# Kernel tuning notes

Hardware: AMD Instinct MI355X
Metric: run time of the kernel (lower is better)

Reference implementation:

```python
import jax, jax.numpy as jnp
import numpy as np

TOP_K = 4  # moe_top_k


def setup_inputs() -> dict:
    key = jax.random.key(0)
    k1, k2 = jax.random.split(key)
    # hidden states [B, S, D]
    x = jax.random.normal(k1, (4, 4096, 6144), dtype=jnp.float32)
    # router weight [D, E] (nnx.Linear kernel, no bias)
    W = jax.random.normal(k2, (6144, 16), dtype=jnp.float32) * 0.02
    return {"x": x, "W": W}


def reference(x, W):
    # logits: [B, S, E] -- promote to fp32 as the module does
    logits = jnp.einsum('bsd,de->bse', x.astype(jnp.float32), W.astype(jnp.float32))
    weights = jax.nn.softmax(logits, axis=-1)
    # top-k expert selection
    top_weights, top_experts = jax.lax.top_k(weights, TOP_K)
    # moe_normalize_expert_weights = 1 -> L1 normalize the selected weights
    top_weights = top_weights / jnp.sum(jnp.abs(top_weights), axis=-1, keepdims=True)
    return (weights.astype(x.dtype), top_weights.astype(x.dtype), top_experts)
```

## Files before the change

kernel.cpp:

```cpp
#include <hip/hip_runtime.h>
#include <cmath>


namespace {
constexpr int TOKENS = 16384;
constexpr int DIM    = 6144;
constexpr int NE     = 16;
constexpr int TOPK   = 4;
constexpr int T_TILE = 64;
constexpr int SUPER  = 128;
constexpr int RS     = 130;
constexpr int RPAD   = 20;
constexpr int TOPW_OFF = TOKENS * NE;
constexpr int EXP_OFF  = TOPW_OFF + TOKENS * TOPK;
}

__device__ __forceinline__ void fma16(float xs, const float* __restrict__ wrow,
                                      float (&ac)[NE]) {
    const float4 w0 = *reinterpret_cast<const float4*>(wrow + 0);
    const float4 w1 = *reinterpret_cast<const float4*>(wrow + 4);
    const float4 w2 = *reinterpret_cast<const float4*>(wrow + 8);
    const float4 w3 = *reinterpret_cast<const float4*>(wrow + 12);
    ac[0]  = fmaf(xs, w0.x, ac[0]);  ac[1]  = fmaf(xs, w0.y, ac[1]);
    ac[2]  = fmaf(xs, w0.z, ac[2]);  ac[3]  = fmaf(xs, w0.w, ac[3]);
    ac[4]  = fmaf(xs, w1.x, ac[4]);  ac[5]  = fmaf(xs, w1.y, ac[5]);
    ac[6]  = fmaf(xs, w1.z, ac[6]);  ac[7]  = fmaf(xs, w1.w, ac[7]);
    ac[8]  = fmaf(xs, w2.x, ac[8]);  ac[9]  = fmaf(xs, w2.y, ac[9]);
    ac[10] = fmaf(xs, w2.z, ac[10]); ac[11] = fmaf(xs, w2.w, ac[11]);
    ac[12] = fmaf(xs, w3.x, ac[12]); ac[13] = fmaf(xs, w3.y, ac[13]);
    ac[14] = fmaf(xs, w3.z, ac[14]); ac[15] = fmaf(xs, w3.w, ac[15]);
}

template <int KSLICES>
__global__ __launch_bounds__(256) void router_partial_kernel(
    const float* __restrict__ x, const float* __restrict__ W,
    float* __restrict__ partial)
{
    constexpr int KS = DIM / KSLICES;
    constexpr int NS = KS / SUPER;

    __shared__ float smem[T_TILE * RS];

    const int tid  = threadIdx.x;
    const int lane = tid & 63;
    const int wv   = tid >> 6;
    const int wvu  = __builtin_amdgcn_readfirstlane(wv);
    const int slice = blockIdx.x % KSLICES;
    const int tile  = blockIdx.x / KSLICES;
    const int t0 = tile * T_TILE;
    const int d0 = slice * KS;

    const int srow = wv * 2 + (lane >> 5);
    const int scol = (lane & 31) * 4;
    const float* xb = x + (size_t)(t0 + srow) * DIM + d0 + scol;

    float acc[NE];
    #pragma unroll
    for (int e = 0; e < NE; ++e) acc[e] = 0.f;

    float4 buf[8];
    #pragma unroll
    for (int i = 0; i < 8; ++i)
        buf[i] = *reinterpret_cast<const float4*>(xb + (size_t)(i * 8) * DIM);

    #pragma unroll 1
    for (int s = 0; s < NS; ++s) {
        #pragma unroll
        for (int i = 0; i < 8; ++i) {
            float* dst = &smem[(size_t)(srow + i * 8) * RS + scol];
            *reinterpret_cast<float2*>(dst)     = make_float2(buf[i].x, buf[i].y);
            *reinterpret_cast<float2*>(dst + 2) = make_float2(buf[i].z, buf[i].w);
        }
        if (s + 1 < NS) {
            const float* xn = xb + (size_t)(s + 1) * SUPER;
            #pragma unroll
            for (int i = 0; i < 8; ++i)
                buf[i] = *reinterpret_cast<const float4*>(xn + (size_t)(i * 8) * DIM);
        }
        __syncthreads();
        {
            const float* xr = &smem[(size_t)lane * RS + wvu * 32];
            const float* wp = W + (size_t)(d0 + s * SUPER + wvu * 32) * NE;
            #pragma unroll
            for (int q = 0; q < 16; ++q) {
                const float2 xq = *reinterpret_cast<const float2*>(xr + 2 * q);
                fma16(xq.x, wp + (2 * q) * NE, acc);
                fma16(xq.y, wp + (2 * q + 1) * NE, acc);
            }
        }
        __syncthreads();
    }

    #pragma unroll
    for (int q = 0; q < 4; ++q)
        *reinterpret_cast<float4*>(&smem[(size_t)(wvu * 64 + lane) * RPAD + 4 * q]) =
            make_float4(acc[4 * q], acc[4 * q + 1], acc[4 * q + 2], acc[4 * q + 3]);
    __syncthreads();

    if (wv == 0) {
        float4 r0[4];
        #pragma unroll
        for (int q = 0; q < 4; ++q)
            r0[q] = *reinterpret_cast<const float4*>(&smem[(size_t)lane * RPAD + 4 * q]);
        #pragma unroll
        for (int w = 1; w < 4; ++w) {
            #pragma unroll
            for (int q = 0; q < 4; ++q) {
                const float4 rw = *reinterpret_cast<const float4*>(
                    &smem[(size_t)(w * 64 + lane) * RPAD + 4 * q]);
                r0[q].x += rw.x; r0[q].y += rw.y; r0[q].z += rw.z; r0[q].w += rw.w;
            }
        }
        float* p = partial + ((size_t)slice * TOKENS + t0 + lane) * NE;
        #pragma unroll
        for (int q = 0; q < 4; ++q)
            *reinterpret_cast<float4*>(p + 4 * q) = r0[q];
    }
}

template <int KSLICES>
__global__ __launch_bounds__(128) void router_finish_kernel(
    const float* __restrict__ partial, float* __restrict__ out)
{
    const int t = blockIdx.x * 128 + threadIdx.x;
    float l[NE];
    {
        const float4* p0 = reinterpret_cast<const float4*>(partial + (size_t)t * NE);
        float4 a0 = p0[0], a1 = p0[1], a2 = p0[2], a3 = p0[3];
        #pragma unroll
        for (int s = 1; s < KSLICES; ++s) {
            const float4* q = reinterpret_cast<const float4*>(
                partial + ((size_t)s * TOKENS + t) * NE);
            float4 b0 = q[0], b1 = q[1], b2 = q[2], b3 = q[3];
            a0.x += b0.x; a0.y += b0.y; a0.z += b0.z; a0.w += b0.w;
            a1.x += b1.x; a1.y += b1.y; a1.z += b1.z; a1.w += b1.w;
            a2.x += b2.x; a2.y += b2.y; a2.z += b2.z; a2.w += b2.w;
            a3.x += b3.x; a3.y += b3.y; a3.z += b3.z; a3.w += b3.w;
        }
        l[0]=a0.x; l[1]=a0.y; l[2]=a0.z; l[3]=a0.w;
        l[4]=a1.x; l[5]=a1.y; l[6]=a1.z; l[7]=a1.w;
        l[8]=a2.x; l[9]=a2.y; l[10]=a2.z; l[11]=a2.w;
        l[12]=a3.x; l[13]=a3.y; l[14]=a3.z; l[15]=a3.w;
    }
    float mx = l[0];
    #pragma unroll
    for (int e = 1; e < NE; ++e) mx = fmaxf(mx, l[e]);
    float w[NE];
    float sum = 0.f;
    #pragma unroll
    for (int e = 0; e < NE; ++e) { w[e] = expf(l[e] - mx); sum += w[e]; }
    const float inv = 1.f / sum;
    #pragma unroll
    for (int e = 0; e < NE; ++e) w[e] *= inv;

    int   idx[TOPK];
    float tw[TOPK];
    unsigned used = 0;
    #pragma unroll
    for (int k = 0; k < TOPK; ++k) {
        float best = -1.f;
        int   bi   = 0;
        #pragma unroll
        for (int e = 0; e < NE; ++e) {
            const bool avail = ((used >> e) & 1u) == 0u;
            if (avail && w[e] > best) { best = w[e]; bi = e; }
        }
        used |= (1u << bi);
        idx[k] = bi;
        tw[k]  = best;
    }
    const float s4 = tw[0] + tw[1] + tw[2] + tw[3];
    const float rinv = 1.f / s4;

    float4* o0 = reinterpret_cast<float4*>(out + (size_t)t * NE);
    o0[0] = make_float4(w[0], w[1], w[2], w[3]);
    o0[1] = make_float4(w[4], w[5], w[6], w[7]);
    o0[2] = make_float4(w[8], w[9], w[10], w[11]);
    o0[3] = make_float4(w[12], w[13], w[14], w[15]);
    *reinterpret_cast<float4*>(out + TOPW_OFF + (size_t)t * TOPK) =
        make_float4(tw[0] * rinv, tw[1] * rinv, tw[2] * rinv, tw[3] * rinv);
    *reinterpret_cast<float4*>(out + EXP_OFF + (size_t)t * TOPK) =
        make_float4((float)idx[0], (float)idx[1], (float)idx[2], (float)idx[3]);
}

template <int KSLICES>
static void launch_impl(const float* x, const float* W, float* out, float* ws,
                        hipStream_t stream)
{
    const int blocks = 256 * KSLICES;
    router_partial_kernel<KSLICES><<<blocks, 256, 0, stream>>>(x, W, ws);
    router_finish_kernel<KSLICES><<<TOKENS / 128, 128, 0, stream>>>(ws, out);
}

extern "C" void kernel_launch(void* const* d_in, const int* in_sizes, int n_in,
                              void* d_out, int out_size, void* d_ws, size_t ws_size,
                              hipStream_t stream) {
    const float* x = (const float*)d_in[0];
    const float* W = (const float*)d_in[1];
    float* out = (float*)d_out;
    float* ws  = (float*)d_ws;

    const size_t per_slice = (size_t)TOKENS * NE * sizeof(float);
    if (ws_size >= 4 * per_slice) {
        launch_impl<4>(x, W, out, ws, stream);
    } else if (ws_size >= 2 * per_slice) {
        launch_impl<2>(x, W, out, ws, stream);
    } else {
        launch_impl<1>(x, W, out, ws, stream);
    }
}
```

Before: 90.10 us.

## Fuse split-K finish into partial kernel via last-block atomic counter

The separate finish kernel is replaced by a per-tile atomic counter, so the last of the four K-slice blocks sums the partials and runs softmax and top-k in the same launch. A small zero-counters kernel is added first. Loads of x become nontemporal to avoid polluting the cache, and the LDS row stride changes from 130 to 134. This relies on threadfence ordering for correctness and still issues two launches.

New measurement: 157.9 us. 1.75x slower.

```diff
diff --git a/kernel.cpp b/kernel.cpp
--- a/kernel.cpp
+++ b/kernel.cpp
@@ -9,10 +9,18 @@
 constexpr int TOPK   = 4;
 constexpr int T_TILE = 64;
 constexpr int SUPER  = 128;
-constexpr int RS     = 130;
+constexpr int RS     = 134;
 constexpr int RPAD   = 20;
+constexpr int KSL    = 4;
+constexpr int NTILES = TOKENS / T_TILE;
 constexpr int TOPW_OFF = TOKENS * NE;
 constexpr int EXP_OFF  = TOPW_OFF + TOKENS * TOPK;
+}
+
+typedef float f4 __attribute__((ext_vector_type(4)));
+
+__device__ __forceinline__ f4 ntload4(const float* p) {
+    return __builtin_nontemporal_load(reinterpret_cast<const f4*>(p));
 }
 
 __device__ __forceinline__ void fma16(float xs, const float* __restrict__ wrow,
@@ -31,22 +39,70 @@
     ac[14] = fmaf(xs, w3.z, ac[14]); ac[15] = fmaf(xs, w3.w, ac[15]);
 }
 
-template <int KSLICES>
-__global__ __launch_bounds__(256) void router_partial_kernel(
+__device__ __forceinline__ void finish_token(const float (&l)[NE], int tt,
+                                             float* __restrict__ out) {
+    float mx = l[0];
+    #pragma unroll
+    for (int e = 1; e < NE; ++e) mx = fmaxf(mx, l[e]);
+    float w[NE];
+    float sum = 0.f;
+    #pragma unroll
+    for (int e = 0; e < NE; ++e) { w[e] = expf(l[e] - mx); sum += w[e]; }
+    const float inv = 1.f / sum;
+    #pragma unroll
+    for (int e = 0; e < NE; ++e) w[e] *= inv;
+
+    int   idx[TOPK];
+    float tw[TOPK];
+    unsigned used = 0;
+    #pragma unroll
+    for (int k = 0; k < TOPK; ++k) {
+        float best = -1.f;
+        int   bi   = 0;
+        #pragma unroll
+        for (int e = 0; e < NE; ++e) {
+            const bool avail = ((used >> e) & 1u) == 0u;
+            if (avail && w[e] > best) { best = w[e]; bi = e; }
+        }
+        used |= (1u << bi);
+        idx[k] = bi;
+        tw[k]  = best;
+    }
+    const float s4 = tw[0] + tw[1] + tw[2] + tw[3];
+    const float rinv = 1.f / s4;
+
+    float4* o0 = reinterpret_cast<float4*>(out + (size_t)tt * NE);
+    o0[0] = make_float4(w[0], w[1], w[2], w[3]);
+    o0[1] = make_float4(w[4], w[5], w[6], w[7]);
+    o0[2] = make_float4(w[8], w[9], w[10], w[11]);
+    o0[3] = make_float4(w[12], w[13], w[14], w[15]);
+    *reinterpret_cast<float4*>(out + TOPW_OFF + (size_t)tt * TOPK) =
+        make_float4(tw[0] * rinv, tw[1] * rinv, tw[2] * rinv, tw[3] * rinv);
+    *reinterpret_cast<float4*>(out + EXP_OFF + (size_t)tt * TOPK) =
+        make_float4((float)idx[0], (float)idx[1], (float)idx[2], (float)idx[3]);
+}
+
+__global__ void zero_counters_kernel(int* __restrict__ cnt) {
+    cnt[threadIdx.x] = 0;
+}
+
+__global__ __launch_bounds__(256) void router_fused_partial_kernel(
     const float* __restrict__ x, const float* __restrict__ W,
-    float* __restrict__ partial)
+    float* __restrict__ partial, int* __restrict__ cnt,
+    float* __restrict__ out)
 {
-    constexpr int KS = DIM / KSLICES;
+    constexpr int KS = DIM / KSL;
     constexpr int NS = KS / SUPER;
 
     __shared__ float smem[T_TILE * RS];
+    __shared__ int sflag;
 
     const int tid  = threadIdx.x;
     const int lane = tid & 63;
     const int wv   = tid >> 6;
     const int wvu  = __builtin_amdgcn_readfirstlane(wv);
-    const int slice = blockIdx.x % KSLICES;
-    const int tile  = blockIdx.x / KSLICES;
+    const int slice = blockIdx.x & 3;
+    const int tile  = blockIdx.x >> 2;
     const int t0 = tile * T_TILE;
     const int d0 = slice * KS;
 
@@ -58,10 +114,10 @@
     #pragma unroll
     for (int e = 0; e < NE; ++e) acc[e] = 0.f;
 
-    float4 buf[8];
+    f4 buf[8];
     #pragma unroll
     for (int i = 0; i < 8; ++i)
-        buf[i] = *reinterpret_cast<const float4*>(xb + (size_t)(i * 8) * DIM);
+        buf[i] = ntload4(xb + (size_t)(i * 8) * DIM);
 
     #pragma unroll 1
     for (int s = 0; s < NS; ++s) {
@@ -75,7 +131,7 @@
             const float* xn = xb + (size_t)(s + 1) * SUPER;
             #pragma unroll
             for (int i = 0; i < 8; ++i)
-                buf[i] = *reinterpret_cast<const float4*>(xn + (size_t)(i * 8) * DIM);
+                buf[i] = ntload4(xn + (size_t)(i * 8) * DIM);
         }
         __syncthreads();
         {
@@ -115,11 +171,113 @@
         #pragma unroll
         for (int q = 0; q < 4; ++q)
             *reinterpret_cast<float4*>(p + 4 * q) = r0[q];
-    }
-}
-
-template <int KSLICES>
-__global__ __launch_bounds__(128) void router_finish_kernel(
+
+        __threadfence();
+        if (lane == 0) sflag = atomicAdd(&cnt[tile], 1);
+    }
+    __syncthreads();
+
+    if (sflag == 3 && tid < T_TILE) {
+        __threadfence();
+        const int t = t0 + tid;
+        float l[NE];
+        {
+            const float4* p0 = reinterpret_cast<const float4*>(partial + (size_t)t * NE);
+            float4 a0 = p0[0], a1 = p0[1], a2 = p0[2], a3 = p0[3];
+            #pragma unroll
+            for (int s = 1; s < KSL; ++s) {
+                const float4* q = reinterpret_cast<const float4*>(
+                    partial + ((size_t)s * TOKENS + t) * NE);
+                float4 b0 = q[0], b1 = q[1], b2 = q[2], b3 = q[3];
+                a0.x += b0.x; a0.y += b0.y; a0.z += b0.z; a0.w += b0.w;
+                a1.x += b1.x; a1.y += b1.y; a1.z += b1.z; a1.w += b1.w;
+                a2.x += b2.x; a2.y += b2.y; a2.z += b2.z; a2.w += b2.w;
+                a3.x += b3.x; a3.y += b3.y; a3.z += b3.z; a3.w += b3.w;
+            }
+            l[0]=a0.x; l[1]=a0.y; l[2]=a0.z; l[3]=a0.w;
+            l[4]=a1.x; l[5]=a1.y; l[6]=a1.z; l[7]=a1.w;
+            l[8]=a2.x; l[9]=a2.y; l[10]=a2.z; l[11]=a2.w;
+            l[12]=a3.x; l[13]=a3.y; l[14]=a3.z; l[15]=a3.w;
+        }
+        finish_token(l, t, out);
+    }
+}
+
+__global__ __launch_bounds__(256) void router_partial_sep_kernel(
+    const float* __restrict__ x, const float* __restrict__ W,
+    float* __restrict__ partial)
+{
+    constexpr int KS = DIM / KSL;
+    constexpr int NS = KS / SUPER;
+    __shared__ float smem[T_TILE * RS];
+    const int tid  = threadIdx.x;
+    const int lane = tid & 63;
+    const int wv   = tid >> 6;
+    const int wvu  = __builtin_amdgcn_readfirstlane(wv);
+    const int slice = blockIdx.x & 3;
+    const int tile  = blockIdx.x >> 2;
+    const int t0 = tile * T_TILE;
+    const int d0 = slice * KS;
+    const int srow = wv * 2 + (lane >> 5);
+    const int scol = (lane & 31) * 4;
+    const float* xb = x + (size_t)(t0 + srow) * DIM + d0 + scol;
+    float acc[NE];
+    #pragma unroll
+    for (int e = 0; e < NE; ++e) acc[e] = 0.f;
+    f4 buf[8];
+    #pragma unroll
+    for (int i = 0; i < 8; ++i) buf[i] = ntload4(xb + (size_t)(i * 8) * DIM);
+    #pragma unroll 1
+    for (int s = 0; s < NS; ++s) {
+        #pragma unroll
+        for (int i = 0; i < 8; ++i) {
+            float* dst = &smem[(size_t)(srow + i * 8) * RS + scol];
+            *reinterpret_cast<float2*>(dst)     = make_float2(buf[i].x, buf[i].y);
+            *reinterpret_cast<float2*>(dst + 2) = make_float2(buf[i].z, buf[i].w);
+        }
+        if (s + 1 < NS) {
+            const float* xn = xb + (size_t)(s + 1) * SUPER;
+            #pragma unroll
+            for (int i = 0; i < 8; ++i) buf[i] = ntload4(xn + (size_t)(i * 8) * DIM);
+        }
+        __syncthreads();
+        {
+            const float* xr = &smem[(size_t)lane * RS + wvu * 32];
+            const float* wp = W + (size_t)(d0 + s * SUPER + wvu * 32) * NE;
+            #pragma unroll
+            for (int q = 0; q < 16; ++q) {
+                const float2 xq = *reinterpret_cast<const float2*>(xr + 2 * q);
+                fma16(xq.x, wp + (2 * q) * NE, acc);
+                fma16(xq.y, wp + (2 * q + 1) * NE, acc);
+            }
+        }
+        __syncthreads();
+    }
+    #pragma unroll
+    for (int q = 0; q < 4; ++q)
+        *reinterpret_cast<float4*>(&smem[(size_t)(wvu * 64 + lane) * RPAD + 4 * q]) =
+            make_float4(acc[4 * q], acc[4 * q + 1], acc[4 * q + 2], acc[4 * q + 3]);
+    __syncthreads();
+    if (wv == 0) {
+        float4 r0[4];
+        #pragma unroll
+        for (int q = 0; q < 4; ++q)
+            r0[q] = *reinterpret_cast<const float4*>(&smem[(size_t)lane * RPAD + 4 * q]);
+        #pragma unroll
+        for (int w = 1; w < 4; ++w)
+            #pragma unroll
+            for (int q = 0; q < 4; ++q) {
+                const float4 rw = *reinterpret_cast<const float4*>(
+                    &smem[(size_t)(w * 64 + lane) * RPAD + 4 * q]);
+                r0[q].x += rw.x; r0[q].y += rw.y; r0[q].z += rw.z; r0[q].w += rw.w;
+            }
+        float* p = partial + ((size_t)slice * TOKENS + t0 + lane) * NE;
+        #pragma unroll
+        for (int q = 0; q < 4; ++q) *reinterpret_cast<float4*>(p + 4 * q) = r0[q];
+    }
+}
+
+__global__ __launch_bounds__(128) void router_finish_sep_kernel(
     const float* __restrict__ partial, float* __restrict__ out)
 {
     const int t = blockIdx.x * 128 + threadIdx.x;
@@ -128,7 +286,7 @@
         const float4* p0 = reinterpret_cast<const float4*>(partial + (size_t)t * NE);
         float4 a0 = p0[0], a1 = p0[1], a2 = p0[2], a3 = p0[3];
         #pragma unroll
-        for (int s = 1; s < KSLICES; ++s) {
+        for (int s = 1; s < KSL; ++s) {
             const float4* q = reinterpret_cast<const float4*>(
                 partial + ((size_t)s * TOKENS + t) * NE);
             float4 b0 = q[0], b1 = q[1], b2 = q[2], b3 = q[3];
@@ -142,54 +300,7 @@
         l[8]=a2.x; l[9]=a2.y; l[10]=a2.z; l[11]=a2.w;
         l[12]=a3.x; l[13]=a3.y; l[14]=a3.z; l[15]=a3.w;
     }
-    float mx = l[0];
-    #pragma unroll
-    for (int e = 1; e < NE; ++e) mx = fmaxf(mx, l[e]);
-    float w[NE];
-    float sum = 0.f;
-    #pragma unroll
-    for (int e = 0; e < NE; ++e) { w[e] = expf(l[e] - mx); sum += w[e]; }
-    const float inv = 1.f / sum;
-    #pragma unroll
-    for (int e = 0; e < NE; ++e) w[e] *= inv;
-
-    int   idx[TOPK];
-    float tw[TOPK];
-    unsigned used = 0;
-    #pragma unroll
-    for (int k = 0; k < TOPK; ++k) {
-        float best = -1.f;
-        int   bi   = 0;
-        #pragma unroll
-        for (int e = 0; e < NE; ++e) {
-            const bool avail = ((used >> e) & 1u) == 0u;
-            if (avail && w[e] > best) { best = w[e]; bi = e; }
-        }
-        used |= (1u << bi);
-        idx[k] = bi;
-        tw[k]  = best;
-    }
-    const float s4 = tw[0] + tw[1] + tw[2] + tw[3];
-    const float rinv = 1.f / s4;
-
-    float4* o0 = reinterpret_cast<float4*>(out + (size_t)t * NE);
-    o0[0] = make_float4(w[0], w[1], w[2], w[3]);
-    o0[1] = make_float4(w[4], w[5], w[6], w[7]);
-    o0[2] = make_float4(w[8], w[9], w[10], w[11]);
-    o0[3] = make_float4(w[12], w[13], w[14], w[15]);
-    *reinterpret_cast<float4*>(out + TOPW_OFF + (size_t)t * TOPK) =
-        make_float4(tw[0] * rinv, tw[1] * rinv, tw[2] * rinv, tw[3] * rinv);
-    *reinterpret_cast<float4*>(out + EXP_OFF + (size_t)t * TOPK) =
-        make_float4((float)idx[0], (float)idx[1], (float)idx[2], (float)idx[3]);
-}
-
-template <int KSLICES>
-static void launch_impl(const float* x, const float* W, float* out, float* ws,
-                        hipStream_t stream)
-{
-    const int blocks = 256 * KSLICES;
-    router_partial_kernel<KSLICES><<<blocks, 256, 0, stream>>>(x, W, ws);
-    router_finish_kernel<KSLICES><<<TOKENS / 128, 128, 0, stream>>>(ws, out);
+    finish_token(l, t, out);
 }
 
 extern "C" void kernel_launch(void* const* d_in, const int* in_sizes, int n_in,
@@ -200,12 +311,15 @@
     float* out = (float*)d_out;
     float* ws  = (float*)d_ws;
 
-    const size_t per_slice = (size_t)TOKENS * NE * sizeof(float);
-    if (ws_size >= 4 * per_slice) {
-        launch_impl<4>(x, W, out, ws, stream);
-    } else if (ws_size >= 2 * per_slice) {
-        launch_impl<2>(x, W, out, ws, stream);
+    const size_t partial_bytes = (size_t)KSL * TOKENS * NE * sizeof(float);
+    const size_t need = partial_bytes + NTILES * sizeof(int);
+
+    if (ws_size >= need) {
+        int* cnt = reinterpret_cast<int*>((char*)d_ws + partial_bytes);
+        zero_counters_kernel<<<1, NTILES, 0, stream>>>(cnt);
+        router_fused_partial_kernel<<<NTILES * KSL, 256, 0, stream>>>(x, W, ws, cnt, out);
     } else {
-        launch_impl<1>(x, W, out, ws, stream);
-    }
-}
+        router_partial_sep_kernel<<<NTILES * KSL, 256, 0, stream>>>(x, W, ws);
+        router_finish_sep_kernel<<<TOKENS / 128, 128, 0, stream>>>(ws, out);
+    }
+}
```

## Give each wave its own token slab to drop block barriers and LDS reduction

Applied to the files above, without the earlier changes.

Each wave now stages and consumes its own 16-token slice of x in a private LDS region, removing both __syncthreads per k-step. Lanes split into 16 tokens by 4 column chunks, and partial sums are combined with cross-lane shuffles instead of an LDS reduction by wave 0. This reduces synchronization stalls and the end-of-block reduction, at the cost of less W broadcast reuse (4 distinct W rows per wave access) and reliance on in-wave lockstep for LDS reuse safety.

After: 312.4 us. 3.47x slower.

```diff
diff --git a/kernel.cpp b/kernel.cpp
--- a/kernel.cpp
+++ b/kernel.cpp
@@ -9,8 +9,7 @@
 constexpr int TOPK   = 4;
 constexpr int T_TILE = 64;
 constexpr int SUPER  = 128;
-constexpr int RS     = 130;
-constexpr int RPAD   = 20;
+constexpr int RS     = 132;
 constexpr int TOPW_OFF = TOKENS * NE;
 constexpr int EXP_OFF  = TOPW_OFF + TOKENS * TOPK;
 }
@@ -31,28 +30,30 @@
     ac[14] = fmaf(xs, w3.z, ac[14]); ac[15] = fmaf(xs, w3.w, ac[15]);
 }
 
-template <int KSLICES>
+template <int KSL>
 __global__ __launch_bounds__(256) void router_partial_kernel(
     const float* __restrict__ x, const float* __restrict__ W,
     float* __restrict__ partial)
 {
-    constexpr int KS = DIM / KSLICES;
+    constexpr int KS = DIM / KSL;
     constexpr int NS = KS / SUPER;
 
-    __shared__ float smem[T_TILE * RS];
+    __shared__ float smem[4][16 * RS];
 
-    const int tid  = threadIdx.x;
-    const int lane = tid & 63;
-    const int wv   = tid >> 6;
-    const int wvu  = __builtin_amdgcn_readfirstlane(wv);
-    const int slice = blockIdx.x % KSLICES;
-    const int tile  = blockIdx.x / KSLICES;
-    const int t0 = tile * T_TILE;
-    const int d0 = slice * KS;
+    const int lane = threadIdx.x & 63;
+    const int wv   = threadIdx.x >> 6;
+    const int slice = blockIdx.x % KSL;
+    const int tile  = blockIdx.x / KSL;
+    const int t0w = tile * T_TILE + wv * 16;
+    const int d0  = slice * KS;
 
-    const int srow = wv * 2 + (lane >> 5);
+    const int srow = lane >> 5;
     const int scol = (lane & 31) * 4;
-    const float* xb = x + (size_t)(t0 + srow) * DIM + d0 + scol;
+    const float* xb = x + (size_t)(t0w + srow) * DIM + d0 + scol;
+    float* wb = &smem[wv][0];
+
+    const int tt = lane & 15;
+    const int m  = lane >> 4;
 
     float acc[NE];
     #pragma unroll
@@ -61,26 +62,22 @@
     float4 buf[8];
     #pragma unroll
     for (int i = 0; i < 8; ++i)
-        buf[i] = *reinterpret_cast<const float4*>(xb + (size_t)(i * 8) * DIM);
+        buf[i] = *reinterpret_cast<const float4*>(xb + (size_t)(2 * i) * DIM);
 
     #pragma unroll 1
     for (int s = 0; s < NS; ++s) {
         #pragma unroll
-        for (int i = 0; i < 8; ++i) {
-            float* dst = &smem[(size_t)(srow + i * 8) * RS + scol];
-            *reinterpret_cast<float2*>(dst)     = make_float2(buf[i].x, buf[i].y);
-            *reinterpret_cast<float2*>(dst + 2) = make_float2(buf[i].z, buf[i].w);
-        }
+        for (int i = 0; i < 8; ++i)
+            *reinterpret_cast<float4*>(&wb[(2 * i + srow) * RS + scol]) = buf[i];
         if (s + 1 < NS) {
             const float* xn = xb + (size_t)(s + 1) * SUPER;
             #pragma unroll
             for (int i = 0; i < 8; ++i)
-                buf[i] = *reinterpret_cast<const float4*>(xn + (size_t)(i * 8) * DIM);
+                buf[i] = *reinterpret_cast<const float4*>(xn + (size_t)(2 * i) * DIM);
         }
-        __syncthreads();
         {
-            const float* xr = &smem[(size_t)lane * RS + wvu * 32];
-            const float* wp = W + (size_t)(d0 + s * SUPER + wvu * 32) * NE;
+            const float* xr = &wb[tt * RS + m * 32];
+            const float* wp = W + (size_t)(d0 + s * SUPER + m * 32) * NE;
             #pragma unroll
             for (int q = 0; q < 16; ++q) {
                 const float2 xq = *reinterpret_cast<const float2*>(xr + 2 * q);
@@ -88,37 +85,22 @@
                 fma16(xq.y, wp + (2 * q + 1) * NE, acc);
             }
         }
-        __syncthreads();
     }
 
     #pragma unroll
-    for (int q = 0; q < 4; ++q)
-        *reinterpret_cast<float4*>(&smem[(size_t)(wvu * 64 + lane) * RPAD + 4 * q]) =
-            make_float4(acc[4 * q], acc[4 * q + 1], acc[4 * q + 2], acc[4 * q + 3]);
-    __syncthreads();
+    for (int e = 0; e < NE; ++e) {
+        float v = acc[e];
+        v += __shfl_xor(v, 16, 64);
+        v += __shfl_xor(v, 32, 64);
+        acc[e] = v;
+    }
 
-    if (wv == 0) {
-        float4 r0[4];
-        #pragma unroll
-        for (int q = 0; q < 4; ++q)
-            r0[q] = *reinterpret_cast<const float4*>(&smem[(size_t)lane * RPAD + 4 * q]);
-        #pragma unroll
-        for (int w = 1; w < 4; ++w) {
-            #pragma unroll
-            for (int q = 0; q < 4; ++q) {
-                const float4 rw = *reinterpret_cast<const float4*>(
-                    &smem[(size_t)(w * 64 + lane) * RPAD + 4 * q]);
-                r0[q].x += rw.x; r0[q].y += rw.y; r0[q].z += rw.z; r0[q].w += rw.w;
-            }
-        }
-        float* p = partial + ((size_t)slice * TOKENS + t0 + lane) * NE;
-        #pragma unroll
-        for (int q = 0; q < 4; ++q)
-            *reinterpret_cast<float4*>(p + 4 * q) = r0[q];
-    }
+    *reinterpret_cast<float4*>(
+        partial + ((size_t)slice * TOKENS + t0w + tt) * NE + m * 4) =
+        make_float4(acc[m * 4], acc[m * 4 + 1], acc[m * 4 + 2], acc[m * 4 + 3]);
 }
 
-template <int KSLICES>
+template <int KSL>
 __global__ __launch_bounds__(128) void router_finish_kernel(
     const float* __restrict__ partial, float* __restrict__ out)
 {
@@ -128,7 +110,7 @@
         const float4* p0 = reinterpret_cast<const float4*>(partial + (size_t)t * NE);
         float4 a0 = p0[0], a1 = p0[1], a2 = p0[2], a3 = p0[3];
         #pragma unroll
-        for (int s = 1; s < KSLICES; ++s) {
+        for (int s = 1; s < KSL; ++s) {
             const float4* q = reinterpret_cast<const float4*>(
                 partial + ((size_t)s * TOKENS + t) * NE);
             float4 b0 = q[0], b1 = q[1], b2 = q[2], b3 = q[3];
@@ -183,13 +165,12 @@
         make_float4((float)idx[0], (float)idx[1], (float)idx[2], (float)idx[3]);
 }
 
-template <int KSLICES>
+template <int KSL>
 static void launch_impl(const float* x, const float* W, float* out, float* ws,
                         hipStream_t stream)
 {
-    const int blocks = 256 * KSLICES;
-    router_partial_kernel<KSLICES><<<blocks, 256, 0, stream>>>(x, W, ws);
-    router_finish_kernel<KSLICES><<<TOKENS / 128, 128, 0, stream>>>(ws, out);
+    router_partial_kernel<KSL><<<(TOKENS / T_TILE) * KSL, 256, 0, stream>>>(x, W, ws);
+    router_finish_kernel<KSL><<<TOKENS / 128, 128, 0, stream>>>(ws, out);
 }
 
 extern "C" void kernel_launch(void* const* d_in, const int* in_sizes, int n_in,
```
